# Kernel tuning notes

Measured on AMD Instinct MI355X. Metric: run time of the kernel, lower is better.

The kernel has to match this reference:

```python
import jax, jax.numpy as jnp
import numpy as np

N = 4096          # nodes (single graph, batch=None)
E = 65536         # edges (avg degree 16)
C = 256           # hidden_channels
L = 3             # num_layers
H = 8             # attention heads
EPS = 1e-5        # batchnorm eps


def setup_inputs() -> dict:
    key = jax.random.key(0)
    ks = iter(jax.random.split(key, 64))
    s = 0.05
    d = {}
    d['x'] = jax.random.normal(next(ks), (N, 1), dtype=jnp.float32)
    d['edge_index'] = jax.random.randint(next(ks), (2, E), 0, N, dtype=jnp.int32)
    # input projection Linear(1, C)
    d['lin1_w'] = jax.random.normal(next(ks), (C, 1), dtype=jnp.float32) * s
    d['lin1_b'] = jnp.zeros((C,), dtype=jnp.float32)
    # GIN MLP: Linear(C,C) -> ReLU -> Linear(C,C), stacked over layers
    d['gin_w1'] = jax.random.normal(next(ks), (L, C, C), dtype=jnp.float32) * s
    d['gin_b1'] = jnp.zeros((L, C), dtype=jnp.float32)
    d['gin_w2'] = jax.random.normal(next(ks), (L, C, C), dtype=jnp.float32) * s
    d['gin_b2'] = jnp.zeros((L, C), dtype=jnp.float32)
    # MultiheadAttention projections
    for nm in ['attn_wq', 'attn_wk', 'attn_wv', 'attn_wo']:
        d[nm] = jax.random.normal(next(ks), (L, C, C), dtype=jnp.float32) * s
    for nm in ['attn_bq', 'attn_bk', 'attn_bv', 'attn_bo']:
        d[nm] = jnp.zeros((L, C), dtype=jnp.float32)
    # three BatchNorms per GPSConv layer
    for nm in ['bn1', 'bn2', 'bn3']:
        d[nm + '_g'] = jnp.ones((L, C), dtype=jnp.float32)
        d[nm + '_b'] = jnp.zeros((L, C), dtype=jnp.float32)
    # GPSConv feedforward: Linear(C, 2C) -> ReLU -> Linear(2C, C)
    d['mlp_w1'] = jax.random.normal(next(ks), (L, 2 * C, C), dtype=jnp.float32) * s
    d['mlp_b1'] = jnp.zeros((L, 2 * C), dtype=jnp.float32)
    d['mlp_w2'] = jax.random.normal(next(ks), (L, C, 2 * C), dtype=jnp.float32) * s
    d['mlp_b2'] = jnp.zeros((L, C), dtype=jnp.float32)
    return d


def _bn(v, g, b):
    # training-mode BatchNorm1d over the node dimension (biased variance)
    m = v.mean(0)
    var = v.var(0)
    return (v - m) * jax.lax.rsqrt(var + EPS) * g + b


def _gps_forward(x, edge_index, lin1_w, lin1_b, gin_w1, gin_b1, gin_w2, gin_b2,
                 attn_wq, attn_bq, attn_wk, attn_bk, attn_wv, attn_bv,
                 attn_wo, attn_bo, bn1_g, bn1_b, bn2_g, bn2_b, bn3_g, bn3_b,
                 mlp_w1, mlp_b1, mlp_w2, mlp_b2):
    h = x @ lin1_w.T + lin1_b                     # [N, C]
    src, dst = edge_index[0], edge_index[1]
    dh = C // H
    scale = 1.0 / jnp.sqrt(jnp.float32(dh))
    for l in range(L):
        xin = h
        # --- GIN branch: gather -> scatter-sum -> MLP ---
        agg = jax.ops.segment_sum(xin[src], dst, num_segments=N)   # [N, C]
        z = xin + agg                                               # eps=0
        z = jax.nn.relu(z @ gin_w1[l].T + gin_b1[l]) @ gin_w2[l].T + gin_b2[l]
        h1 = _bn(z + xin, bn1_g[l], bn1_b[l])
        # --- global multihead attention over all N nodes ---
        q = (xin @ attn_wq[l].T + attn_bq[l]).reshape(N, H, dh)
        k = (xin @ attn_wk[l].T + attn_bk[l]).reshape(N, H, dh)
        v = (xin @ attn_wv[l].T + attn_bv[l]).reshape(N, H, dh)
        scores = jnp.einsum('nhd,mhd->hnm', q, k) * scale           # [H, N, N]
        a = jax.nn.softmax(scores, axis=-1)
        o = jnp.einsum('hnm,mhd->nhd', a, v).reshape(N, C)
        o = o @ attn_wo[l].T + attn_bo[l]
        h2 = _bn(o + xin, bn2_g[l], bn2_b[l])
        # --- combine + feedforward ---
        s = h1 + h2
        m = jax.nn.relu(s @ mlp_w1[l].T + mlp_b1[l]) @ mlp_w2[l].T + mlp_b2[l]
        h = _bn(s + m, bn3_g[l], bn3_b[l])
    return h


def reference(x, edge_index, lin1_w, lin1_b, gin_w1, gin_b1, gin_w2, gin_b2,
              attn_wq, attn_bq, attn_wk, attn_bk, attn_wv, attn_bv,
              attn_wo, attn_bo, bn1_g, bn1_b, bn2_g, bn2_b, bn3_g, bn3_b,
              mlp_w1, mlp_b1, mlp_w2, mlp_b2):
    return _gps_forward(x, edge_index, lin1_w, lin1_b, gin_w1, gin_b1, gin_w2,
                        gin_b2, attn_wq, attn_bq, attn_wk, attn_bk, attn_wv,
                        attn_bv, attn_wo, attn_bo, bn1_g, bn1_b, bn2_g, bn2_b,
                        bn3_g, bn3_b, mlp_w1, mlp_b1, mlp_w2, mlp_b2)
```

## Files before the change

kernel.cpp:

```cpp
#include <hip/hip_runtime.h>

#define NN 4096
#define NE 65536
#define C 256
#define NL 3
#define NH 8
#define DH 32
#define EPS 1e-5f
#define SPLIT 2
#define KT8 (NN/128/SPLIT)
#define ATTN_BLKS ((NN/128)*NH*SPLIT)
#define VS 136

typedef __bf16 bf16x8 __attribute__((ext_vector_type(8)));
typedef __bf16 bf16x4v __attribute__((ext_vector_type(4)));
typedef float f32x4 __attribute__((ext_vector_type(4)));
typedef short bf16x4s __attribute__((ext_vector_type(4)));

#define QSCALE (0.17677669529663687f * 1.4426950408889634f)

#define CC1 (C*C)
#define GS 72

__global__ __launch_bounds__(256) void prep_w(const float* __restrict__ s0,
        const float* __restrict__ s1, const float* __restrict__ s2,
        const float* __restrict__ s3, const float* __restrict__ s4,
        const float* __restrict__ s5, const float* __restrict__ s6,
        const float* __restrict__ s7, __bf16* __restrict__ dst) {
    int g = blockIdx.y;
    int i = (blockIdx.x*256 + threadIdx.x)*4;
    const float* src; int n;
    switch (g) {
        case 0: src=s0; n=3*CC1; break;
        case 1: src=s1; n=3*CC1; break;
        case 2: src=s2; n=3*CC1; break;
        case 3: src=s3; n=3*CC1; break;
        case 4: src=s4; n=3*CC1; break;
        case 5: src=s5; n=3*CC1; break;
        case 6: src=s6; n=6*CC1; break;
        default: src=s7; n=6*CC1; break;
    }
    if (i >= n) return;
    size_t off;
    if (g >= 2 && g <= 4) {
        int l = i >> 16, rem = i & (CC1-1);
        off = (size_t)(6 + 3*l + (g-2))*CC1 + rem;
    } else {
        size_t base = (g==0) ? 0 : (g==1) ? 3*(size_t)CC1 : (g==5) ? 15*(size_t)CC1
                    : (g==6) ? 18*(size_t)CC1 : 24*(size_t)CC1;
        off = base + i;
    }
    float4 t = *(const float4*)(src + i);
    bf16x4v o = {(__bf16)t.x, (__bf16)t.y, (__bf16)t.z, (__bf16)t.w};
    *(bf16x4v*)(dst + off) = o;
}

__global__ __launch_bounds__(256) void lin1_kernel(const float* __restrict__ x,
        const float* __restrict__ w, const float* __restrict__ b,
        __bf16* __restrict__ out) {
    int n = blockIdx.x, c = threadIdx.x;
    out[(size_t)n*C + c] = (__bf16)(x[n]*w[c] + b[c]);
}

__global__ __launch_bounds__(256) void hist_kernel(const int* __restrict__ ei,
        int* __restrict__ cnt) {
    int e = blockIdx.x*256 + threadIdx.x;
    atomicAdd(&cnt[ei[NE + e]], 1);
}

__global__ __launch_bounds__(256) void scan_kernel(const int* __restrict__ cnt,
        int* __restrict__ rowptr, int* __restrict__ cursor) {
    __shared__ int tot[256];
    __shared__ int pre[257];
    int t = threadIdx.x;
    int base = t*16;
    int local[16];
    int s = 0;
    #pragma unroll
    for (int i = 0; i < 16; i++) { local[i] = s; s += cnt[base+i]; }
    tot[t] = s;
    __syncthreads();
    if (t == 0) {
        int acc = 0;
        for (int i = 0; i < 256; i++) { pre[i] = acc; acc += tot[i]; }
        pre[256] = acc;
    }
    __syncthreads();
    int off = pre[t];
    #pragma unroll
    for (int i = 0; i < 16; i++) {
        rowptr[base+i] = off + local[i];
        cursor[base+i] = off + local[i];
    }
    if (t == 0) rowptr[NN] = pre[256];
}

__global__ __launch_bounds__(256) void fill_kernel(const int* __restrict__ ei,
        int* __restrict__ cursor, int* __restrict__ eidsrc) {
    int e = blockIdx.x*256 + threadIdx.x;
    int dst = ei[NE + e], src = ei[e];
    int pos = atomicAdd(&cursor[dst], 1);
    eidsrc[pos] = src;
}

template<int QKV, int BN, int COMB>
__device__ __forceinline__ void gemm_core(int bm, int bn,
        const __bf16* A, const float* A2f, const __bf16* A2b, const __bf16* W,
        const float* b0, const float* b1, const float* b2,
        const __bf16* add1, const __bf16* add2,
        __bf16* out, __bf16* vt, __bf16* ktp, float* stats,
        const float* coefs,
        const float* st1, const float* g1, const float* bb1,
        const float* st2, const float* g2, const float* bb2,
        const float* lsum,
        int K, int Nout, int relu, __bf16* As, __bf16* Ws) {
    int tid = threadIdx.x;
    int wave = tid >> 6, lane = tid & 63;
    int ln = lane & 15, quad = lane >> 4;
    int row = tid >> 2, kseg = (tid & 3) * 16;
    f32x4 acc[4] = {};
    for (int k0 = 0; k0 < K; k0 += 64) {
        __syncthreads();
        {
            bf16x8 a0, a1;
            if constexpr (COMB) {
                int rowg = bm + row;
                int head = (k0 + kseg) >> 5;
                float w[SPLIT];
                float tot = 0.f;
                #pragma unroll
                for (int zz = 0; zz < SPLIT; zz++) {
                    w[zz] = lsum[((size_t)zz*NH + head)*NN + rowg];
                    tot += w[zz];
                }
                float inv = 1.0f / tot;
                float v[16] = {};
                #pragma unroll
                for (int zz = 0; zz < SPLIT; zz++) {
                    const __bf16* p = &A[((size_t)zz*NN + rowg)*C + k0 + kseg];
                    bf16x8 x0 = *(const bf16x8*)p, x1 = *(const bf16x8*)(p + 8);
                    #pragma unroll
                    for (int j = 0; j < 8; j++) {
                        v[j]   += w[zz]*(float)x0[j];
                        v[8+j] += w[zz]*(float)x1[j];
                    }
                }
                #pragma unroll
                for (int j = 0; j < 8; j++) {
                    a0[j] = (__bf16)(v[j]*inv);
                    a1[j] = (__bf16)(v[8+j]*inv);
                }
            } else {
                const __bf16* ap = &A[(size_t)(bm+row)*K + k0 + kseg];
                a0 = *(const bf16x8*)ap;
                a1 = *(const bf16x8*)(ap + 8);
                if constexpr (BN == 1) {
                    const __bf16* p = &A2b[(size_t)(bm+row)*K + k0 + kseg];
                    bf16x8 z0 = *(const bf16x8*)p;
                    bf16x8 z1v = *(const bf16x8*)(p + 8);
                    float sc1[16], sh1[16], sc2[16], sh2[16];
                    #pragma unroll
                    for (int i = 0; i < 4; i++) {
                        *(float4*)&sc1[i*4] = *(const float4*)&coefs[k0 + kseg + i*4];
                        *(float4*)&sh1[i*4] = *(const float4*)&coefs[C + k0 + kseg + i*4];
                        *(float4*)&sc2[i*4] = *(const float4*)&coefs[2*C + k0 + kseg + i*4];
                        *(float4*)&sh2[i*4] = *(const float4*)&coefs[3*C + k0 + kseg + i*4];
                    }
                    #pragma unroll
                    for (int j = 0; j < 8; j++) {
                        a0[j] = (__bf16)((float)a0[j]*sc1[j] + sh1[j]
                                       + (float)z0[j]*sc2[j] + sh2[j]);
                        a1[j] = (__bf16)((float)a1[j]*sc1[8+j] + sh1[8+j]
                                       + (float)z1v[j]*sc2[8+j] + sh2[8+j]);
                    }
                } else if (A2f) {
                    const float* p = &A2f[(size_t)(bm+row)*K + k0 + kseg];
                    float4 t0 = *(const float4*)p;
                    float4 t1 = *(const float4*)(p+4);
                    float4 t2 = *(const float4*)(p+8);
                    float4 t3 = *(const float4*)(p+12);
                    a0[0]=(__bf16)((float)a0[0]+t0.x); a0[1]=(__bf16)((float)a0[1]+t0.y);
                    a0[2]=(__bf16)((float)a0[2]+t0.z); a0[3]=(__bf16)((float)a0[3]+t0.w);
                    a0[4]=(__bf16)((float)a0[4]+t1.x); a0[5]=(__bf16)((float)a0[5]+t1.y);
                    a0[6]=(__bf16)((float)a0[6]+t1.z); a0[7]=(__bf16)((float)a0[7]+t1.w);
                    a1[0]=(__bf16)((float)a1[0]+t2.x); a1[1]=(__bf16)((float)a1[1]+t2.y);
                    a1[2]=(__bf16)((float)a1[2]+t2.z); a1[3]=(__bf16)((float)a1[3]+t2.w);
                    a1[4]=(__bf16)((float)a1[4]+t3.x); a1[5]=(__bf16)((float)a1[5]+t3.y);
                    a1[6]=(__bf16)((float)a1[6]+t3.z); a1[7]=(__bf16)((float)a1[7]+t3.w);
                }
            }
            *(bf16x8*)&As[row*GS + kseg]     = a0;
            *(bf16x8*)&As[row*GS + kseg + 8] = a1;
            const __bf16* wp = &W[(size_t)(bn+row)*K + k0 + kseg];
            *(bf16x8*)&Ws[row*GS + kseg]     = *(const bf16x8*)wp;
            *(bf16x8*)&Ws[row*GS + kseg + 8] = *(const bf16x8*)(wp + 8);
        }
        __syncthreads();
        #pragma unroll
        for (int kt2 = 0; kt2 < 2; kt2++) {
            bf16x8 bfr = *(const bf16x8*)&Ws[(wave*16+ln)*GS + kt2*32 + quad*8];
            #pragma unroll
            for (int i = 0; i < 4; i++) {
                bf16x8 afr = *(const bf16x8*)&As[(i*16+ln)*GS + kt2*32 + quad*8];
                acc[i] = __builtin_amdgcn_mfma_f32_16x16x32_bf16(afr, bfr, acc[i], 0, 0, 0);
            }
        }
    }
    int col = bn + wave*16 + ln;
    if constexpr (QKV) {
        float bsv = col < 256 ? b0[col] : (col < 512 ? b1[col-256] : b2[col-512]);
        if (col < 256) {
            #pragma unroll
            for (int i = 0; i < 4; i++)
                #pragma unroll
                for (int rr = 0; rr < 4; rr++)
                    out[(size_t)(bm + i*16 + quad*4 + rr)*C + col] =
                        (__bf16)((acc[i][rr] + bsv) * (float)QSCALE);
        } else if (col < 512) {
            int hd = (col-256) >> 5, dh = (col-256) & 31;
            #pragma unroll
            for (int i = 0; i < 4; i++)
                #pragma unroll
                for (int rr = 0; rr < 4; rr++)
                    ktp[((size_t)hd*NN + bm + i*16 + quad*4 + rr)*DH + dh] =
                        (__bf16)(acc[i][rr] + bsv);
        } else {
            int vrow = col - 512;
            #pragma unroll
            for (int i = 0; i < 4; i++) {
                bf16x4v pk = {(__bf16)(acc[i][0]+bsv), (__bf16)(acc[i][1]+bsv),
                              (__bf16)(acc[i][2]+bsv), (__bf16)(acc[i][3]+bsv)};
                *(bf16x4v*)&vt[(size_t)vrow*NN + bm + i*16 + quad*4] = pk;
            }
        }
        return;
    }
    float bsv = b0[col];
    float sc1 = 0.f, sh1 = 0.f, sc2 = 0.f, sh2 = 0.f;
    if constexpr (BN == 2) {
        float m1 = st1[col]*(1.f/NN);
        sc1 = rsqrtf(st1[C+col]*(1.f/NN) - m1*m1 + EPS) * g1[col];
        sh1 = bb1[col] - m1*sc1;
        float m2 = st2[col]*(1.f/NN);
        sc2 = rsqrtf(st2[C+col]*(1.f/NN) - m2*m2 + EPS) * g2[col];
        sh2 = bb2[col] - m2*sc2;
    }
    float ssum = 0.f, ssq = 0.f;
    #pragma unroll
    for (int i = 0; i < 4; i++) {
        #pragma unroll
        for (int rr = 0; rr < 4; rr++) {
            int rw = bm + i*16 + quad*4 + rr;
            float vv = acc[i][rr] + bsv;
            if (relu) vv = fmaxf(vv, 0.f);
            size_t idx = (size_t)rw*Nout + col;
            if constexpr (BN == 2) {
                vv += (float)add1[idx]*sc1 + sh1 + (float)add2[idx]*sc2 + sh2;
            } else {
                if (add1) vv += (float)add1[idx];
                if (add2) vv += (float)add2[idx];
            }
            out[idx] = (__bf16)vv;
            ssum += vv; ssq += vv*vv;
        }
    }
    if (stats) {
        ssum += __shfl_xor(ssum, 16); ssum += __shfl_xor(ssum, 32);
        ssq  += __shfl_xor(ssq, 16);  ssq  += __shfl_xor(ssq, 32);
        if (quad == 0) {
            atomicAdd(&stats[col], ssum);
            atomicAdd(&stats[Nout + col], ssq);
        }
    }
}

__device__ __forceinline__ void attn_body(int t, const __bf16* __restrict__ qbuf,
        const __bf16* __restrict__ kt, const __bf16* __restrict__ vt,
        __bf16* __restrict__ opart, float* __restrict__ lsum, __bf16* lds) {
    int head = t & 7, z = t >> 8, qb = ((t >> 3) & 31) * 128;
    int hb = head * DH;
    int tid = threadIdx.x;
    int wave = tid >> 6, lane = tid & 63;
    int ln = lane & 15, quad = lane >> 4;
    __bf16* Kb0 = lds;
    __bf16* Kb1 = lds + 4608;
    __bf16* Vb0 = lds + 9216;
    __bf16* Vb1 = lds + 9216 + 32*VS;

    bf16x8 qf[2];
    #pragma unroll
    for (int g = 0; g < 2; g++)
        qf[g] = *(const bf16x8*)&qbuf[(size_t)(qb + wave*32 + g*16 + ln)*C + hb + quad*8];

    f32x4 ot[2][2] = {};
    f32x4 la[2] = {};
    const bf16x4s ones = {(short)0x3F80, (short)0x3F80, (short)0x3F80, (short)0x3F80};

    int srow = tid >> 1, sseg = (tid & 1) * 16;
    int vd = tid >> 3, vseg = (tid & 7) * 16;
    int kt0 = z * KT8;
    const __bf16* kbase = &kt[(size_t)head*NN*DH];
    {
        const __bf16* kp = &kbase[(size_t)(kt0*128 + srow)*DH + sseg];
        *(bf16x8*)&Kb0[srow*36 + sseg]     = *(const bf16x8*)kp;
        *(bf16x8*)&Kb0[srow*36 + sseg + 8] = *(const bf16x8*)(kp + 8);
        const __bf16* vp = &vt[(size_t)(hb + vd)*NN + kt0*128 + vseg];
        *(bf16x8*)&Vb0[vd*VS + vseg]     = *(const bf16x8*)vp;
        *(bf16x8*)&Vb0[vd*VS + vseg + 8] = *(const bf16x8*)(vp + 8);
    }
    for (int i = 0; i < KT8; i++) {
        int kb = (kt0 + i) * 128;
        __bf16* Kc = (i & 1) ? Kb1 : Kb0;
        __bf16* Kn = (i & 1) ? Kb0 : Kb1;
        __bf16* Vc = (i & 1) ? Vb1 : Vb0;
        __bf16* Vn = (i & 1) ? Vb0 : Vb1;
        __syncthreads();
        bf16x8 nk0, nk1, nv0, nv1;
        bool hasNext = (i + 1 < KT8);
        if (hasNext) {
            const __bf16* kp = &kbase[(size_t)(kb + 128 + srow)*DH + sseg];
            nk0 = *(const bf16x8*)kp;
            nk1 = *(const bf16x8*)(kp + 8);
            const __bf16* vp = &vt[(size_t)(hb + vd)*NN + kb + 128 + vseg];
            nv0 = *(const bf16x8*)vp;
            nv1 = *(const bf16x8*)(vp + 8);
        }
        #pragma unroll
        for (int pr = 0; pr < 4; pr++) {
            bf16x8 kf0 = *(const bf16x8*)&Kc[((pr*2+0)*16+ln)*36 + quad*8];
            bf16x8 kf1 = *(const bf16x8*)&Kc[((pr*2+1)*16+ln)*36 + quad*8];
            bf16x4s vf[2][2];
            #pragma unroll
            for (int s = 0; s < 2; s++)
                #pragma unroll
                for (int h = 0; h < 2; h++)
                    vf[s][h] = *(const bf16x4s*)&Vc[(h*16+ln)*VS + (pr*2+s)*16 + quad*4];
            f32x4 zz = {0.f,0.f,0.f,0.f};
            f32x4 st00 = __builtin_amdgcn_mfma_f32_16x16x32_bf16(kf0, qf[0], zz, 0, 0, 0);
            f32x4 st10 = __builtin_amdgcn_mfma_f32_16x16x32_bf16(kf0, qf[1], zz, 0, 0, 0);
            f32x4 st01 = __builtin_amdgcn_mfma_f32_16x16x32_bf16(kf1, qf[0], zz, 0, 0, 0);
            f32x4 st11 = __builtin_amdgcn_mfma_f32_16x16x32_bf16(kf1, qf[1], zz, 0, 0, 0);
            union { __bf16 b[4]; bf16x4s s; } pf00, pf01, pf10, pf11;
            #pragma unroll
            for (int rr = 0; rr < 4; rr++) {
                pf00.b[rr] = (__bf16)__builtin_amdgcn_exp2f(st00[rr]);
                pf01.b[rr] = (__bf16)__builtin_amdgcn_exp2f(st01[rr]);
                pf10.b[rr] = (__bf16)__builtin_amdgcn_exp2f(st10[rr]);
                pf11.b[rr] = (__bf16)__builtin_amdgcn_exp2f(st11[rr]);
            }
            ot[0][0] = __builtin_amdgcn_mfma_f32_16x16x16bf16_1k(vf[0][0], pf00.s, ot[0][0], 0, 0, 0);
            ot[0][1] = __builtin_amdgcn_mfma_f32_16x16x16bf16_1k(vf[0][1], pf00.s, ot[0][1], 0, 0, 0);
            ot[1][0] = __builtin_amdgcn_mfma_f32_16x16x16bf16_1k(vf[0][0], pf10.s, ot[1][0], 0, 0, 0);
            ot[1][1] = __builtin_amdgcn_mfma_f32_16x16x16bf16_1k(vf[0][1], pf10.s, ot[1][1], 0, 0, 0);
            la[0]    = __builtin_amdgcn_mfma_f32_16x16x16bf16_1k(ones,     pf00.s, la[0],    0, 0, 0);
            la[1]    = __builtin_amdgcn_mfma_f32_16x16x16bf16_1k(ones,     pf10.s, la[1],    0, 0, 0);
            ot[0][0] = __builtin_amdgcn_mfma_f32_16x16x16bf16_1k(vf[1][0], pf01.s, ot[0][0], 0, 0, 0);
            ot[0][1] = __builtin_amdgcn_mfma_f32_16x16x16bf16_1k(vf[1][1], pf01.s, ot[0][1], 0, 0, 0);
            ot[1][0] = __builtin_amdgcn_mfma_f32_16x16x16bf16_1k(vf[1][0], pf11.s, ot[1][0], 0, 0, 0);
            ot[1][1] = __builtin_amdgcn_mfma_f32_16x16x16bf16_1k(vf[1][1], pf11.s, ot[1][1], 0, 0, 0);
            la[0]    = __builtin_amdgcn_mfma_f32_16x16x16bf16_1k(ones,     pf01.s, la[0],    0, 0, 0);
            la[1]    = __builtin_amdgcn_mfma_f32_16x16x16bf16_1k(ones,     pf11.s, la[1],    0, 0, 0);
        }
        if (hasNext) {
            *(bf16x8*)&Kn[srow*36 + sseg]     = nk0;
            *(bf16x8*)&Kn[srow*36 + sseg + 8] = nk1;
            *(bf16x8*)&Vn[vd*VS + vseg]     = nv0;
            *(bf16x8*)&Vn[vd*VS + vseg + 8] = nv1;
        }
    }
    #pragma unroll
    for (int g = 0; g < 2; g++) {
        float l_ = la[g][0];
        float inv = 1.0f / l_;
        int qrow = qb + wave*32 + g*16 + ln;
        #pragma unroll
        for (int h = 0; h < 2; h++) {
            bf16x4v pk = {(__bf16)(ot[g][h][0]*inv), (__bf16)(ot[g][h][1]*inv),
                          (__bf16)(ot[g][h][2]*inv), (__bf16)(ot[g][h][3]*inv)};
            *(bf16x4v*)&opart[((size_t)z*NN + qrow)*C + hb + h*16 + quad*4] = pk;
        }
        if (quad == 0)
            lsum[((size_t)z*NH + head)*NN + qrow] = l_;
    }
}

__global__ __launch_bounds__(256) void qkv_agg_kernel(const __bf16* __restrict__ Hb,
        const __bf16* __restrict__ Wqkv, const float* __restrict__ bq,
        const float* __restrict__ bk, const float* __restrict__ bv,
        __bf16* __restrict__ qout, __bf16* __restrict__ ktout,
        __bf16* __restrict__ vtout,
        const int* __restrict__ rowptr, const int* __restrict__ eidsrc,
        float* __restrict__ agg) {
    __shared__ __bf16 lds[9216];
    int bx = blockIdx.x;
    if (bx < 768) {
        gemm_core<1,0,0>((bx & 63)*64, (bx >> 6)*64, Hb, nullptr, nullptr, Wqkv,
                bq, bk, bv, nullptr, nullptr, qout, vtout, ktout, nullptr,
                nullptr, nullptr, nullptr, nullptr, nullptr, nullptr, nullptr,
                nullptr, C, 768, 0, lds, lds + 4608);
        return;
    }
    int tid = threadIdx.x;
    int wave = tid >> 6, lane = tid & 63;
    int node = (bx - 768)*4 + wave;
    int beg = rowptr[node], end = rowptr[node+1];
    float s0 = 0.f, s1 = 0.f, s2 = 0.f, s3 = 0.f;
    for (int e = beg; e < end; e++) {
        int src = eidsrc[e];
        bf16x4v hv = *(const bf16x4v*)&Hb[(size_t)src*C + lane*4];
        s0 += (float)hv[0]; s1 += (float)hv[1];
        s2 += (float)hv[2]; s3 += (float)hv[3];
    }
    float4 o = {s0, s1, s2, s3};
    *(float4*)&agg[(size_t)node*C + lane*4] = o;
}

__global__ __launch_bounds__(256) void gin1_attn_kernel(const __bf16* __restrict__ Hb,
        const float* __restrict__ agg, const __bf16* __restrict__ gw1,
        const float* __restrict__ gb1, __bf16* __restrict__ t1,
        const __bf16* __restrict__ qbuf, const __bf16* __restrict__ kt,
        const __bf16* __restrict__ vt,
        __bf16* __restrict__ opart, float* __restrict__ lsum) {
    __shared__ __bf16 lds[17920];
    int bx = blockIdx.x;
    if (bx < 256) {
        gemm_core<0,0,0>((bx >> 2)*64, (bx & 3)*64, Hb, agg, nullptr, gw1,
                gb1, nullptr, nullptr, nullptr, nullptr, t1, nullptr, nullptr,
                nullptr, nullptr, nullptr, nullptr, nullptr, nullptr, nullptr,
                nullptr, nullptr, C, C, 1, lds, lds + 4608);
        return;
    }
    attn_body(bx - 256, qbuf, kt, vt, opart, lsum, lds);
}

__global__ __launch_bounds__(256) void gin2_proj_kernel(const __bf16* __restrict__ t1,
        const __bf16* __restrict__ gw2, const float* __restrict__ gb2,
        const __bf16* __restrict__ Hb, __bf16* __restrict__ z1, float* __restrict__ st1,
        const __bf16* __restrict__ opart, const float* __restrict__ lsum,
        const __bf16* __restrict__ wop, const float* __restrict__ lbo,
        __bf16* __restrict__ z2, float* __restrict__ st2) {
    __shared__ __bf16 lds[9216];
    int bx = blockIdx.x;
    if (bx < 256) {
        gemm_core<0,0,0>((bx >> 2)*64, (bx & 3)*64, t1, nullptr, nullptr, gw2,
                gb2, nullptr, nullptr, Hb, nullptr, z1, nullptr, nullptr, st1,
                nullptr, nullptr, nullptr, nullptr, nullptr, nullptr, nullptr,
                nullptr, C, C, 0, lds, lds + 4608);
        return;
    }
    int t = bx - 256;
    gemm_core<0,0,1>((t >> 2)*64, (t & 3)*64, opart, nullptr, nullptr, wop,
            lbo, nullptr, nullptr, Hb, nullptr, z2, nullptr, nullptr, st2,
            nullptr, nullptr, nullptr, nullptr, nullptr, nullptr, nullptr,
            lsum, C, C, 0, lds, lds + 4608);
}

__global__ __launch_bounds__(256) void ff1_kernel(const __bf16* __restrict__ z1,
        const __bf16* __restrict__ z2, const __bf16* __restrict__ mw1,
        const float* __restrict__ lmb1, __bf16* __restrict__ hidden,
        const float* __restrict__ st1, const float* __restrict__ g1,
        const float* __restrict__ bb1, const float* __restrict__ st2,
        const float* __restrict__ g2, const float* __restrict__ bb2) {
    __shared__ __bf16 lds[9216];
    __shared__ float coefs[4*C];
    int tid = threadIdx.x;
    {
        float m = st1[tid]*(1.f/NN);
        float var = st1[C+tid]*(1.f/NN) - m*m;
        float s = rsqrtf(var + EPS) * g1[tid];
        coefs[tid] = s; coefs[C+tid] = bb1[tid] - m*s;
        m = st2[tid]*(1.f/NN);
        var = st2[C+tid]*(1.f/NN) - m*m;
        s = rsqrtf(var + EPS) * g2[tid];
        coefs[2*C+tid] = s; coefs[3*C+tid] = bb2[tid] - m*s;
    }
    int bx = blockIdx.x;
    gemm_core<0,1,0>((bx >> 3)*64, (bx & 7)*64, z1, nullptr, z2, mw1,
            lmb1, nullptr, nullptr, nullptr, nullptr, hidden, nullptr, nullptr,
            nullptr, coefs, nullptr, nullptr, nullptr, nullptr, nullptr, nullptr,
            nullptr, C, 2*C, 1, lds, lds + 4608);
}

__global__ __launch_bounds__(256) void ff2_kernel(const __bf16* __restrict__ hidden,
        const __bf16* __restrict__ mw2, const float* __restrict__ lmb2,
        const __bf16* __restrict__ z1, const __bf16* __restrict__ z2,
        __bf16* __restrict__ zbuf3, float* __restrict__ st3,
        const float* __restrict__ st1, const float* __restrict__ g1,
        const float* __restrict__ bb1, const float* __restrict__ st2,
        const float* __restrict__ g2, const float* __restrict__ bb2) {
    __shared__ __bf16 lds[9216];
    int bx = blockIdx.x;
    gemm_core<0,2,0>((bx >> 2)*64, (bx & 3)*64, hidden, nullptr, nullptr, mw2,
            lmb2, nullptr, nullptr, z1, z2, zbuf3, nullptr, nullptr, st3,
            nullptr, st1, g1, bb1, st2, g2, bb2,
            nullptr, 2*C, C, 0, lds, lds + 4608);
}

__global__ __launch_bounds__(256) void bn_apply_kernel(const __bf16* __restrict__ z,
        const float* __restrict__ stats, const float* __restrict__ g,
        const float* __restrict__ b, __bf16* __restrict__ outb,
        float* __restrict__ outf) {
    int idx4 = (blockIdx.x*256 + threadIdx.x) * 4;
    int c = idx4 & (C-1);
    bf16x4v zv = *(const bf16x4v*)&z[idx4];
    float4 st = *(const float4*)&stats[c];
    float4 sq = *(const float4*)&stats[C + c];
    float4 gv = *(const float4*)&g[c];
    float4 bv = *(const float4*)&b[c];
    float o[4];
    float m0 = st.x*(1.f/NN), m1 = st.y*(1.f/NN), m2 = st.z*(1.f/NN), m3 = st.w*(1.f/NN);
    o[0] = ((float)zv[0] - m0) * rsqrtf(sq.x*(1.f/NN) - m0*m0 + EPS) * gv.x + bv.x;
    o[1] = ((float)zv[1] - m1) * rsqrtf(sq.y*(1.f/NN) - m1*m1 + EPS) * gv.y + bv.y;
    o[2] = ((float)zv[2] - m2) * rsqrtf(sq.z*(1.f/NN) - m2*m2 + EPS) * gv.z + bv.z;
    o[3] = ((float)zv[3] - m3) * rsqrtf(sq.w*(1.f/NN) - m3*m3 + EPS) * gv.w + bv.w;
    if (outb) {
        bf16x4v ov = {(__bf16)o[0], (__bf16)o[1], (__bf16)o[2], (__bf16)o[3]};
        *(bf16x4v*)&outb[idx4] = ov;
    } else {
        float4 ov = {o[0], o[1], o[2], o[3]};
        *(float4*)&outf[idx4] = ov;
    }
}

extern "C" void kernel_launch(void* const* d_in, const int* in_sizes, int n_in,
                              void* d_out, int out_size, void* d_ws, size_t ws_size,
                              hipStream_t stream) {
    const float* x      = (const float*)d_in[0];
    const int*   ei     = (const int*)d_in[1];
    const float* lin1_w = (const float*)d_in[2];
    const float* lin1_b = (const float*)d_in[3];
    const float* gin_w1 = (const float*)d_in[4];
    const float* gin_b1 = (const float*)d_in[5];
    const float* gin_w2 = (const float*)d_in[6];
    const float* gin_b2 = (const float*)d_in[7];
    const float* wq = (const float*)d_in[8];
    const float* wk = (const float*)d_in[9];
    const float* wv = (const float*)d_in[10];
    const float* wo = (const float*)d_in[11];
    const float* bq = (const float*)d_in[12];
    const float* bk = (const float*)d_in[13];
    const float* bv = (const float*)d_in[14];
    const float* bo = (const float*)d_in[15];
    const float* bn1_g = (const float*)d_in[16];
    const float* bn1_b = (const float*)d_in[17];
    const float* bn2_g = (const float*)d_in[18];
    const float* bn2_b = (const float*)d_in[19];
    const float* bn3_g = (const float*)d_in[20];
    const float* bn3_b = (const float*)d_in[21];
    const float* mw1 = (const float*)d_in[22];
    const float* mb1 = (const float*)d_in[23];
    const float* mw2 = (const float*)d_in[24];
    const float* mb2 = (const float*)d_in[25];

    const size_t MB = 1u << 20;
    char* ws = (char*)d_ws;
    __bf16* Hb      = (__bf16*)(ws);
    __bf16* z1      = (__bf16*)(ws + 2*MB);
    __bf16* zbuf3   = (__bf16*)(ws + 4*MB);
    __bf16* z2      = (__bf16*)(ws + 6*MB);
    __bf16* t1      = (__bf16*)(ws + 8*MB);
    __bf16* Qbuf    = (__bf16*)(ws + 10*MB);
    __bf16* Ktb     = (__bf16*)(ws + 12*MB);
    __bf16* Vt      = (__bf16*)(ws + 14*MB);
    float*  agg     = (float*)(ws + 16*MB);
    __bf16* hiddenb = (__bf16*)(ws + 16*MB);
    __bf16* Opart   = (__bf16*)(ws + 20*MB);
    __bf16* Wb      = (__bf16*)(ws + 28*MB);
    float*  stats   = (float*)(ws + 32*MB);
    int*    cursor  = (int*)(ws + 32*MB + 64*1024);
    int*    rowptr  = (int*)(ws + 32*MB + 96*1024);
    int*    eidsrc  = (int*)(ws + 32*MB + 128*1024);
    float*  lsum    = (float*)(ws + 33*MB);

    dim3 blk(256);

    prep_w<<<dim3(384, 8), blk, 0, stream>>>(gin_w1, gin_w2, wq, wk, wv, wo, mw1, mw2, Wb);
    hipMemsetAsync(stats, 0, 9 * 2 * C * sizeof(float), stream);
    lin1_kernel<<<NN, blk, 0, stream>>>(x, lin1_w, lin1_b, Hb);
    hipMemsetAsync(cursor, 0, NN * sizeof(int), stream);
    hist_kernel<<<NE/256, blk, 0, stream>>>(ei, cursor);
    scan_kernel<<<1, blk, 0, stream>>>(cursor, rowptr, cursor);
    fill_kernel<<<NE/256, blk, 0, stream>>>(ei, cursor, eidsrc);

    for (int l = 0; l < NL; l++) {
        const __bf16* gw1b = Wb + (size_t)l*CC1;
        const __bf16* gw2b = Wb + (size_t)(3+l)*CC1;
        const __bf16* wqkv = Wb + (size_t)(6+3*l)*CC1;
        const __bf16* wop  = Wb + (size_t)(15+l)*CC1;
        const __bf16* mw1p = Wb + (size_t)(18+2*l)*CC1;
        const __bf16* mw2p = Wb + (size_t)(24+2*l)*CC1;
        const float* gb1 = gin_b1 + (size_t)l*C;
        const float* gb2 = gin_b2 + (size_t)l*C;
        const float* lbq = bq + (size_t)l*C;
        const float* lbk = bk + (size_t)l*C;
        const float* lbv = bv + (size_t)l*C;
        const float* lbo = bo + (size_t)l*C;
        const float* lmb1 = mb1 + (size_t)l*2*C;
        const float* lmb2 = mb2 + (size_t)l*C;
        float* st1 = stats + (size_t)l*3*2*C;
        float* st2 = st1 + 2*C;
        float* st3 = st2 + 2*C;
        const float* g1v = bn1_g + (size_t)l*C; const float* b1v = bn1_b + (size_t)l*C;
        const float* g2v = bn2_g + (size_t)l*C; const float* b2v = bn2_b + (size_t)l*C;

        qkv_agg_kernel<<<768 + NN/4, blk, 0, stream>>>(Hb, wqkv, lbq, lbk, lbv,
                Qbuf, Ktb, Vt, rowptr, eidsrc, agg);
        gin1_attn_kernel<<<256 + ATTN_BLKS, blk, 0, stream>>>(Hb, agg,
                gw1b, gb1, t1, Qbuf, Ktb, Vt, Opart, lsum);
        gin2_proj_kernel<<<512, blk, 0, stream>>>(t1, gw2b, gb2, Hb, z1, st1,
                Opart, lsum, wop, lbo, z2, st2);
        ff1_kernel<<<512, blk, 0, stream>>>(z1, z2, mw1p, lmb1, hiddenb,
                st1, g1v, b1v, st2, g2v, b2v);
        ff2_kernel<<<256, blk, 0, stream>>>(hiddenb, mw2p, lmb2, z1, z2,
                zbuf3, st3, st1, g1v, b1v, st2, g2v, b2v);
        if (l == NL-1)
            bn_apply_kernel<<<NN/4, blk, 0, stream>>>(zbuf3, st3,
                    bn3_g + (size_t)l*C, bn3_b + (size_t)l*C, nullptr, (float*)d_out);
        else
            bn_apply_kernel<<<NN/4, blk, 0, stream>>>(zbuf3, st3,
                    bn3_g + (size_t)l*C, bn3_b + (size_t)l*C, Hb, nullptr);
    }
}
```

Measured before the change: 435.0 us.

## Software-pipeline attention QK/PV MFMAs, stagger KV tile order, add setprio

Restructures the attention inner loop so the QK^T MFMAs for the next 32-key sub-block are issued before the exp2 and PV MFMAs of the current one, with LDS fragment loads double-buffered in registers. Each query block also starts at a different KV tile (rotated by its query index) to spread concurrent global reads across blocks. s_setprio brackets the MFMA groups, and the fused gin1/attention kernel gets a launch_bounds occupancy hint of 2. This aims to hide exp and LDS latency behind matrix work, in exchange for higher register pressure that the occupancy hint may force into spills.

```diff
diff --git a/kernel.cpp b/kernel.cpp
--- a/kernel.cpp
+++ b/kernel.cpp
@@ -277,7 +277,7 @@
 __device__ __forceinline__ void attn_body(int t, const __bf16* __restrict__ qbuf,
         const __bf16* __restrict__ kt, const __bf16* __restrict__ vt,
         __bf16* __restrict__ opart, float* __restrict__ lsum, __bf16* lds) {
-    int head = t & 7, z = t >> 8, qb = ((t >> 3) & 31) * 128;
+    int head = t & 7, z = t >> 8, qi = (t >> 3) & 31, qb = qi * 128;
     int hb = head * DH;
     int tid = threadIdx.x;
     int wave = tid >> 6, lane = tid & 63;
@@ -295,71 +295,98 @@
     f32x4 ot[2][2] = {};
     f32x4 la[2] = {};
     const bf16x4s ones = {(short)0x3F80, (short)0x3F80, (short)0x3F80, (short)0x3F80};
+    const f32x4 zz = {0.f,0.f,0.f,0.f};
 
     int srow = tid >> 1, sseg = (tid & 1) * 16;
     int vd = tid >> 3, vseg = (tid & 7) * 16;
     int kt0 = z * KT8;
     const __bf16* kbase = &kt[(size_t)head*NN*DH];
     {
-        const __bf16* kp = &kbase[(size_t)(kt0*128 + srow)*DH + sseg];
+        int i0 = qi & (KT8-1);
+        const __bf16* kp = &kbase[(size_t)((kt0+i0)*128 + srow)*DH + sseg];
         *(bf16x8*)&Kb0[srow*36 + sseg]     = *(const bf16x8*)kp;
         *(bf16x8*)&Kb0[srow*36 + sseg + 8] = *(const bf16x8*)(kp + 8);
-        const __bf16* vp = &vt[(size_t)(hb + vd)*NN + kt0*128 + vseg];
+        const __bf16* vp = &vt[(size_t)(hb + vd)*NN + (kt0+i0)*128 + vseg];
         *(bf16x8*)&Vb0[vd*VS + vseg]     = *(const bf16x8*)vp;
         *(bf16x8*)&Vb0[vd*VS + vseg + 8] = *(const bf16x8*)(vp + 8);
     }
-    for (int i = 0; i < KT8; i++) {
-        int kb = (kt0 + i) * 128;
-        __bf16* Kc = (i & 1) ? Kb1 : Kb0;
-        __bf16* Kn = (i & 1) ? Kb0 : Kb1;
-        __bf16* Vc = (i & 1) ? Vb1 : Vb0;
-        __bf16* Vn = (i & 1) ? Vb0 : Vb1;
+    for (int ii = 0; ii < KT8; ii++) {
+        int inext = (ii + 1 + qi) & (KT8-1);
+        __bf16* Kc = (ii & 1) ? Kb1 : Kb0;
+        __bf16* Kn = (ii & 1) ? Kb0 : Kb1;
+        __bf16* Vc = (ii & 1) ? Vb1 : Vb0;
+        __bf16* Vn = (ii & 1) ? Vb0 : Vb1;
         __syncthreads();
         bf16x8 nk0, nk1, nv0, nv1;
-        bool hasNext = (i + 1 < KT8);
+        bool hasNext = (ii + 1 < KT8);
         if (hasNext) {
-            const __bf16* kp = &kbase[(size_t)(kb + 128 + srow)*DH + sseg];
+            const __bf16* kp = &kbase[(size_t)((kt0+inext)*128 + srow)*DH + sseg];
             nk0 = *(const bf16x8*)kp;
             nk1 = *(const bf16x8*)(kp + 8);
-            const __bf16* vp = &vt[(size_t)(hb + vd)*NN + kb + 128 + vseg];
+            const __bf16* vp = &vt[(size_t)(hb + vd)*NN + (kt0+inext)*128 + vseg];
             nv0 = *(const bf16x8*)vp;
             nv1 = *(const bf16x8*)(vp + 8);
         }
+        bf16x8 kfr[2][2];
+        bf16x4s vfr[2][2][2];
+        f32x4 stq[2][4];
+        kfr[0][0] = *(const bf16x8*)&Kc[((0*16)+ln)*36 + quad*8];
+        kfr[0][1] = *(const bf16x8*)&Kc[((1*16)+ln)*36 + quad*8];
+        stq[0][0] = __builtin_amdgcn_mfma_f32_16x16x32_bf16(kfr[0][0], qf[0], zz, 0, 0, 0);
+        stq[0][1] = __builtin_amdgcn_mfma_f32_16x16x32_bf16(kfr[0][0], qf[1], zz, 0, 0, 0);
+        stq[0][2] = __builtin_amdgcn_mfma_f32_16x16x32_bf16(kfr[0][1], qf[0], zz, 0, 0, 0);
+        stq[0][3] = __builtin_amdgcn_mfma_f32_16x16x32_bf16(kfr[0][1], qf[1], zz, 0, 0, 0);
+        kfr[1][0] = *(const bf16x8*)&Kc[((2*16)+ln)*36 + quad*8];
+        kfr[1][1] = *(const bf16x8*)&Kc[((3*16)+ln)*36 + quad*8];
+        #pragma unroll
+        for (int s = 0; s < 2; s++)
+            #pragma unroll
+            for (int h = 0; h < 2; h++)
+                vfr[0][s][h] = *(const bf16x4s*)&Vc[(h*16+ln)*VS + s*16 + quad*4];
         #pragma unroll
         for (int pr = 0; pr < 4; pr++) {
-            bf16x8 kf0 = *(const bf16x8*)&Kc[((pr*2+0)*16+ln)*36 + quad*8];
-            bf16x8 kf1 = *(const bf16x8*)&Kc[((pr*2+1)*16+ln)*36 + quad*8];
-            bf16x4s vf[2][2];
-            #pragma unroll
-            for (int s = 0; s < 2; s++)
+            const int cur = pr & 1, nxt = cur ^ 1;
+            if (pr < 2) {
+                kfr[cur][0] = *(const bf16x8*)&Kc[(((pr+2)*2+0)*16+ln)*36 + quad*8];
+                kfr[cur][1] = *(const bf16x8*)&Kc[(((pr+2)*2+1)*16+ln)*36 + quad*8];
+            }
+            if (pr < 3) {
                 #pragma unroll
-                for (int h = 0; h < 2; h++)
-                    vf[s][h] = *(const bf16x4s*)&Vc[(h*16+ln)*VS + (pr*2+s)*16 + quad*4];
-            f32x4 zz = {0.f,0.f,0.f,0.f};
-            f32x4 st00 = __builtin_amdgcn_mfma_f32_16x16x32_bf16(kf0, qf[0], zz, 0, 0, 0);
-            f32x4 st10 = __builtin_amdgcn_mfma_f32_16x16x32_bf16(kf0, qf[1], zz, 0, 0, 0);
-            f32x4 st01 = __builtin_amdgcn_mfma_f32_16x16x32_bf16(kf1, qf[0], zz, 0, 0, 0);
-            f32x4 st11 = __builtin_amdgcn_mfma_f32_16x16x32_bf16(kf1, qf[1], zz, 0, 0, 0);
+                for (int s = 0; s < 2; s++)
+                    #pragma unroll
+                    for (int h = 0; h < 2; h++)
+                        vfr[nxt][s][h] = *(const bf16x4s*)&Vc[(h*16+ln)*VS + ((pr+1)*2+s)*16 + quad*4];
+            }
+            if (pr < 3) {
+                __builtin_amdgcn_s_setprio(1);
+                stq[nxt][0] = __builtin_amdgcn_mfma_f32_16x16x32_bf16(kfr[nxt][0], qf[0], zz, 0, 0, 0);
+                stq[nxt][1] = __builtin_amdgcn_mfma_f32_16x16x32_bf16(kfr[nxt][0], qf[1], zz, 0, 0, 0);
+                stq[nxt][2] = __builtin_amdgcn_mfma_f32_16x16x32_bf16(kfr[nxt][1], qf[0], zz, 0, 0, 0);
+                stq[nxt][3] = __builtin_amdgcn_mfma_f32_16x16x32_bf16(kfr[nxt][1], qf[1], zz, 0, 0, 0);
+                __builtin_amdgcn_s_setprio(0);
+            }
             union { __bf16 b[4]; bf16x4s s; } pf00, pf01, pf10, pf11;
             #pragma unroll
             for (int rr = 0; rr < 4; rr++) {
-                pf00.b[rr] = (__bf16)__builtin_amdgcn_exp2f(st00[rr]);
-                pf01.b[rr] = (__bf16)__builtin_amdgcn_exp2f(st01[rr]);
-                pf10.b[rr] = (__bf16)__builtin_amdgcn_exp2f(st10[rr]);
-                pf11.b[rr] = (__bf16)__builtin_amdgcn_exp2f(st11[rr]);
-            }
-            ot[0][0] = __builtin_amdgcn_mfma_f32_16x16x16bf16_1k(vf[0][0], pf00.s, ot[0][0], 0, 0, 0);
-            ot[0][1] = __builtin_amdgcn_mfma_f32_16x16x16bf16_1k(vf[0][1], pf00.s, ot[0][1], 0, 0, 0);
-            ot[1][0] = __builtin_amdgcn_mfma_f32_16x16x16bf16_1k(vf[0][0], pf10.s, ot[1][0], 0, 0, 0);
-            ot[1][1] = __builtin_amdgcn_mfma_f32_16x16x16bf16_1k(vf[0][1], pf10.s, ot[1][1], 0, 0, 0);
-            la[0]    = __builtin_amdgcn_mfma_f32_16x16x16bf16_1k(ones,     pf00.s, la[0],    0, 0, 0);
-            la[1]    = __builtin_amdgcn_mfma_f32_16x16x16bf16_1k(ones,     pf10.s, la[1],    0, 0, 0);
-            ot[0][0] = __builtin_amdgcn_mfma_f32_16x16x16bf16_1k(vf[1][0], pf01.s, ot[0][0], 0, 0, 0);
-            ot[0][1] = __builtin_amdgcn_mfma_f32_16x16x16bf16_1k(vf[1][1], pf01.s, ot[0][1], 0, 0, 0);
-            ot[1][0] = __builtin_amdgcn_mfma_f32_16x16x16bf16_1k(vf[1][0], pf11.s, ot[1][0], 0, 0, 0);
-            ot[1][1] = __builtin_amdgcn_mfma_f32_16x16x16bf16_1k(vf[1][1], pf11.s, ot[1][1], 0, 0, 0);
-            la[0]    = __builtin_amdgcn_mfma_f32_16x16x16bf16_1k(ones,     pf01.s, la[0],    0, 0, 0);
-            la[1]    = __builtin_amdgcn_mfma_f32_16x16x16bf16_1k(ones,     pf11.s, la[1],    0, 0, 0);
+                pf00.b[rr] = (__bf16)__builtin_amdgcn_exp2f(stq[cur][0][rr]);
+                pf10.b[rr] = (__bf16)__builtin_amdgcn_exp2f(stq[cur][1][rr]);
+                pf01.b[rr] = (__bf16)__builtin_amdgcn_exp2f(stq[cur][2][rr]);
+                pf11.b[rr] = (__bf16)__builtin_amdgcn_exp2f(stq[cur][3][rr]);
+            }
+            __builtin_amdgcn_s_setprio(1);
+            ot[0][0] = __builtin_amdgcn_mfma_f32_16x16x16bf16_1k(vfr[cur][0][0], pf00.s, ot[0][0], 0, 0, 0);
+            ot[0][1] = __builtin_amdgcn_mfma_f32_16x16x16bf16_1k(vfr[cur][0][1], pf00.s, ot[0][1], 0, 0, 0);
+            ot[1][0] = __builtin_amdgcn_mfma_f32_16x16x16bf16_1k(vfr[cur][0][0], pf10.s, ot[1][0], 0, 0, 0);
+            ot[1][1] = __builtin_amdgcn_mfma_f32_16x16x16bf16_1k(vfr[cur][0][1], pf10.s, ot[1][1], 0, 0, 0);
+            la[0]    = __builtin_amdgcn_mfma_f32_16x16x16bf16_1k(ones, pf00.s, la[0], 0, 0, 0);
+            la[1]    = __builtin_amdgcn_mfma_f32_16x16x16bf16_1k(ones, pf10.s, la[1], 0, 0, 0);
+            ot[0][0] = __builtin_amdgcn_mfma_f32_16x16x16bf16_1k(vfr[cur][1][0], pf01.s, ot[0][0], 0, 0, 0);
+            ot[0][1] = __builtin_amdgcn_mfma_f32_16x16x16bf16_1k(vfr[cur][1][1], pf01.s, ot[0][1], 0, 0, 0);
+            ot[1][0] = __builtin_amdgcn_mfma_f32_16x16x16bf16_1k(vfr[cur][1][0], pf11.s, ot[1][0], 0, 0, 0);
+            ot[1][1] = __builtin_amdgcn_mfma_f32_16x16x16bf16_1k(vfr[cur][1][1], pf11.s, ot[1][1], 0, 0, 0);
+            la[0]    = __builtin_amdgcn_mfma_f32_16x16x16bf16_1k(ones, pf01.s, la[0], 0, 0, 0);
+            la[1]    = __builtin_amdgcn_mfma_f32_16x16x16bf16_1k(ones, pf11.s, la[1], 0, 0, 0);
+            __builtin_amdgcn_s_setprio(0);
         }
         if (hasNext) {
             *(bf16x8*)&Kn[srow*36 + sseg]     = nk0;
@@ -415,7 +442,7 @@
     *(float4*)&agg[(size_t)node*C + lane*4] = o;
 }
 
-__global__ __launch_bounds__(256) void gin1_attn_kernel(const __bf16* __restrict__ Hb,
+__global__ __launch_bounds__(256, 2) void gin1_attn_kernel(const __bf16* __restrict__ Hb,
         const float* __restrict__ agg, const __bf16* __restrict__ gw1,
         const float* __restrict__ gb1, __bf16* __restrict__ t1,
         const __bf16* __restrict__ qbuf, const __bf16* __restrict__ kt,
```

Measured after the change: 432.9 us. About the same (-0.5%).
